# Optimization experiments

Measured on AMD Instinct MI355X. Metric: run time of the kernel, lower is better.

The kernel has to match this reference:

```python
import jax, jax.numpy as jnp
import numpy as np

E = 256
H = 8
DH = E // H
N = 200000
NEG = -1e9


def _normalize(x, eps=1e-12):
    # torch F.normalize: x / max(||x||_2, eps) along last dim
    n = jnp.linalg.norm(x, axis=-1, keepdims=True)
    return x / jnp.maximum(n, eps)


def setup_inputs() -> dict:
    key = jax.random.key(0)
    ks = jax.random.split(key, 16)
    s = 1.0 / np.sqrt(E)
    inp = {
        "context_vector": jax.random.normal(ks[0], (3 * E,), jnp.float32),
        "node_embeddings": jax.random.normal(ks[1], (N, E), jnp.float32),
        "invalid_action_mask": jax.random.randint(ks[2], (N,), 0, 2).astype(bool),
        # project_context: Linear(3E, E)
        "Wc": jax.random.normal(ks[3], (E, 3 * E), jnp.float32) * (1.0 / np.sqrt(3 * E)),
        "bc": jnp.zeros((E,), jnp.float32),
        # project_keys / project_values: Linear(E, E)
        "Wk": jax.random.normal(ks[4], (E, E), jnp.float32) * s,
        "bk": jnp.zeros((E,), jnp.float32),
        "Wv": jax.random.normal(ks[5], (E, E), jnp.float32) * s,
        "bv": jnp.zeros((E,), jnp.float32),
        # nn.MultiheadAttention packed in-projection and out-projection
        "in_proj_w": jax.random.normal(ks[6], (3 * E, E), jnp.float32) * s,
        "in_proj_b": jnp.zeros((3 * E,), jnp.float32),
        "out_proj_w": jax.random.normal(ks[7], (E, E), jnp.float32) * s,
        "out_proj_b": jnp.zeros((E,), jnp.float32),
        # project_attn_output: Linear(E, E)
        "Wo": jax.random.normal(ks[8], (E, E), jnp.float32) * s,
        "bo": jnp.zeros((E,), jnp.float32),
    }
    # guarantee at least one valid action
    inp["invalid_action_mask"] = inp["invalid_action_mask"].at[0].set(False)
    return inp


def reference(context_vector, node_embeddings, invalid_action_mask,
              Wc, bc, Wk, bk, Wv, bv,
              in_proj_w, in_proj_b, out_proj_w, out_proj_b, Wo, bo):
    valid = ~invalid_action_mask                        # [N]

    query = context_vector @ Wc.T + bc                  # [E]
    keys = _normalize(node_embeddings @ Wk.T + bk)      # [N, E]
    values = _normalize(node_embeddings @ Wv.T + bv)    # [N, E]

    # MultiheadAttention, single query, batch 1
    wq, wk2, wv2 = in_proj_w[:E], in_proj_w[E:2 * E], in_proj_w[2 * E:]
    bq, bk2, bv2 = in_proj_b[:E], in_proj_b[E:2 * E], in_proj_b[2 * E:]
    q = (query @ wq.T + bq).reshape(H, DH)              # [H, DH]
    k = (keys @ wk2.T + bk2).reshape(N, H, DH)          # [N, H, DH]
    v = (values @ wv2.T + bv2).reshape(N, H, DH)

    logits = jnp.einsum("hd,nhd->hn", q, k) / np.sqrt(DH)   # [H, N]
    logits = jnp.where(valid[None, :], logits, NEG)
    w = jax.nn.softmax(logits, axis=-1)                 # [H, N]
    attn = jnp.einsum("hn,nhd->hd", w, v).reshape(E)    # [E]
    attn = attn @ out_proj_w.T + out_proj_b             # [E]

    attn = _normalize(attn @ Wo.T + bo)                 # [E]

    # pointer scores over valid nodes (invalid -> prob 0)
    scores = jnp.where(valid, keys @ attn, NEG)         # [N]
    probs = jax.nn.softmax(scores)                      # [N]
    return probs
```

## Files before the change

### kernel.cpp

```cpp
#include <hip/hip_runtime.h>

#define NN 200000
#define NEGV -1000000000.0f

typedef __attribute__((ext_vector_type(8))) short bf16x8;
typedef __attribute__((ext_vector_type(4))) float f32x4;

__device__ __forceinline__ float bf2f(unsigned short u){
  unsigned int x = ((unsigned int)u) << 16;
  return __builtin_bit_cast(float, x);
}
__device__ __forceinline__ unsigned short f2bf(float f){
  unsigned int x = __builtin_bit_cast(unsigned int, f);
  x += 0x7fffu + ((x >> 16) & 1u);
  return (unsigned short)(x >> 16);
}
__device__ __forceinline__ void gload16(const void* g, void* l){
  __builtin_amdgcn_global_load_lds((const __attribute__((address_space(1))) unsigned int*)g,
                                   (__attribute__((address_space(3))) unsigned int*)l, 16, 0, 0);
}

static constexpr size_t OFF_RK     = 0;
static constexpr size_t OFF_RV     = 800256;
static constexpr size_t OFF_LOGITS = 1600512;
static constexpr size_t OFF_SCORES = 8000512;
static constexpr size_t OFF_QUERY  = 8800768;
static constexpr size_t OFF_Q2     = 8801792;
static constexpr size_t OFF_A2     = 8802816;
static constexpr size_t OFF_CONSTS = 8811008;
static constexpr size_t OFF_BIMG   = 8811264;
static constexpr size_t OFF_LSTAT  = 9081600;
static constexpr size_t OFF_MZ     = 9089792;
static constexpr size_t OFF_KATTN  = 9089856;
static constexpr size_t OFF_KB     = 9090880;
static constexpr size_t OFF_UPART  = 9090944;
static constexpr size_t OFF_TPART  = 13285248;
static constexpr size_t OFF_U      = 13301632;
static constexpr size_t OFF_T      = 13309824;
static constexpr size_t OFF_P3STAT = 13309888;
static constexpr size_t OFF_MZ3    = 13313984;
static constexpr size_t OFF_EMBBF  = 13314048;
static constexpr size_t WS_NEED_BF = OFF_EMBBF + (size_t)NN*512;

__global__ void k_query(const float* __restrict__ ctx, const float* __restrict__ Wc,
                        const float* __restrict__ bc, float* __restrict__ query){
  int e = blockIdx.x, t = threadIdx.x;
  float p = 0.f;
  #pragma unroll
  for (int r = 0; r < 3; r++){ int j = r*256 + t; p += ctx[j] * Wc[e*768 + j]; }
  #pragma unroll
  for (int m = 32; m; m >>= 1) p += __shfl_xor(p, m);
  __shared__ float red[4];
  if ((t & 63) == 0) red[t >> 6] = p;
  __syncthreads();
  if (t == 0) query[e] = red[0] + red[1] + red[2] + red[3] + bc[e];
}

__global__ void k_q2(const float* __restrict__ query, const float* __restrict__ ipw,
                     const float* __restrict__ ipb, float* __restrict__ q2){
  int d = blockIdx.x, t = threadIdx.x;
  float p = query[t] * ipw[d*256 + t];
  #pragma unroll
  for (int m = 32; m; m >>= 1) p += __shfl_xor(p, m);
  __shared__ float red[4];
  if ((t & 63) == 0) red[t >> 6] = p;
  __syncthreads();
  if (t == 0) q2[d] = red[0] + red[1] + red[2] + red[3] + ipb[d];
}

__global__ void k_AA(const float* __restrict__ q2, const float* __restrict__ ipw,
                     const float* __restrict__ ipb, const float* __restrict__ Wk,
                     const float* __restrict__ bk, float* __restrict__ A2,
                     float* __restrict__ consts){
  int h = blockIdx.x, t = threadIdx.x;
  __shared__ float qs[32];
  __shared__ float AHs[256];
  __shared__ float red[4];
  if (t < 32) qs[t] = q2[h*32 + t];
  __syncthreads();
  float a = 0.f;
  #pragma unroll
  for (int d = 0; d < 32; d++) a += qs[d] * ipw[(256 + h*32 + d)*256 + t];
  AHs[t] = a;
  if (t == 0){
    float ck = 0.f;
    for (int d = 0; d < 32; d++) ck += qs[d] * ipb[256 + h*32 + d];
    consts[8 + h] = ck;
  }
  __syncthreads();
  float a2 = 0.f;
  for (int e = 0; e < 256; e++) a2 += AHs[e] * Wk[e*256 + t];
  A2[h*256 + t] = a2;
  float cc = AHs[t] * bk[t];
  #pragma unroll
  for (int m = 32; m; m >>= 1) cc += __shfl_xor(cc, m);
  if ((t & 63) == 0) red[t >> 6] = cc;
  __syncthreads();
  if (t == 0) consts[h] = red[0] + red[1] + red[2] + red[3];
}

__global__ void k_bimg(const float* __restrict__ Wk, const float* __restrict__ Wv,
                       const float* __restrict__ A2, unsigned char* __restrict__ bimg){
  int g = blockIdx.x*256 + threadIdx.x;
  if (g >= 8*528*4) return;
  int s = g / (528*4);
  int rem = g % (528*4);
  int col = rem >> 2, kg = rem & 3;
  int j0 = s*32 + kg*8;
  const float* src = nullptr;
  if (col < 256) src = Wk + col*256 + j0;
  else if (col < 512) src = Wv + (col-256)*256 + j0;
  else if (col < 520) src = A2 + (col-512)*256 + j0;
  unsigned short u[8];
  #pragma unroll
  for (int i = 0; i < 8; i++) u[i] = src ? f2bf(src[i]) : (unsigned short)0;
  uint4 o;
  o.x = (unsigned int)u[0] | ((unsigned int)u[1] << 16);
  o.y = (unsigned int)u[2] | ((unsigned int)u[3] << 16);
  o.z = (unsigned int)u[4] | ((unsigned int)u[5] << 16);
  o.w = (unsigned int)u[6] | ((unsigned int)u[7] << 16);
  unsigned int addr = (unsigned int)((col*64 + kg*16) ^ ((col & 7) << 4));
  *(uint4*)(bimg + (size_t)s*33792 + addr) = o;
}

__launch_bounds__(256, 2)
__global__ void k_main(const float* __restrict__ emb, const unsigned char* __restrict__ bimg,
                       const int* __restrict__ mask, const float* __restrict__ consts,
                       float* __restrict__ rk_g, float* __restrict__ rv_g,
                       float* __restrict__ logits, unsigned char* __restrict__ ebf){
  __shared__ __align__(16) unsigned char smA[2][4096];
  __shared__ __align__(16) unsigned char smB[2][33792];
  __shared__ float sc_norm[4][64];
  __shared__ float rkbuf[64];
  const int tid = threadIdx.x;
  const int lane = tid & 63, wave = tid >> 6;
  const int c = lane & 15, kg = lane >> 4;
  const int nb0 = blockIdx.x * 64;

  auto stage = [&](int s, int buf){
    const unsigned char* bsrc = bimg + (size_t)s*33792;
    #pragma unroll
    for (int it = 0; it < 9; it++){
      int chunk = it*4 + wave;
      if (chunk < 33)
        gload16(bsrc + chunk*1024 + lane*16, &smB[buf][chunk*1024]);
    }
    int nl = tid >> 2, akg = tid & 3;
    const float* ap = emb + (size_t)(nb0 + nl)*256 + s*32 + akg*8;
    float4 f0 = *(const float4*)ap;
    float4 f1 = *(const float4*)(ap + 4);
    uint4 o;
    o.x = (unsigned int)f2bf(f0.x) | ((unsigned int)f2bf(f0.y) << 16);
    o.y = (unsigned int)f2bf(f0.z) | ((unsigned int)f2bf(f0.w) << 16);
    o.z = (unsigned int)f2bf(f1.x) | ((unsigned int)f2bf(f1.y) << 16);
    o.w = (unsigned int)f2bf(f1.z) | ((unsigned int)f2bf(f1.w) << 16);
    *(uint4*)&smA[buf][nl*64 + ((akg ^ ((nl >> 1) & 3)) << 4)] = o;
    if (ebf) *(uint4*)(ebf + (size_t)(nb0 + nl)*512 + s*64 + akg*16) = o;
  };

  f32x4 acc[4][9];
  #pragma unroll
  for (int st = 0; st < 4; st++)
    #pragma unroll
    for (int f = 0; f < 9; f++) acc[st][f] = (f32x4){0.f,0.f,0.f,0.f};

  stage(0, 0);
  for (int s = 0; s < 8; s++){
    int cur = s & 1;
    __syncthreads();
    if (s < 7) stage(s + 1, cur ^ 1);
    bf16x8 af[4];
    #pragma unroll
    for (int st = 0; st < 4; st++)
      af[st] = *(const bf16x8*)&smA[cur][st*1024 + c*64 + ((kg ^ ((c >> 1) & 3)) << 4)];
    #pragma unroll
    for (int f = 0; f < 9; f++){
      int cf = (f < 8) ? (wave*8 + f) : 32;
      bf16x8 bf = *(const bf16x8*)&smB[cur][(((cf*16 + c)*64 + kg*16)) ^ ((c & 7) << 4)];
      #pragma unroll
      for (int st = 0; st < 4; st++)
        acc[st][f] = __builtin_amdgcn_mfma_f32_16x16x32_bf16(af[st], bf, acc[st][f], 0, 0, 0);
    }
  }

  #pragma unroll
  for (int st = 0; st < 4; st++){
    #pragma unroll
    for (int i = 0; i < 4; i++){
      float p = 0.f;
      #pragma unroll
      for (int f = 0; f < 8; f++) p += acc[st][f][i]*acc[st][f][i];
      #pragma unroll
      for (int m = 1; m < 16; m <<= 1) p += __shfl_xor(p, m);
      if (c == 0) sc_norm[wave][st*16 + kg*4 + i] = p;
    }
  }
  __syncthreads();
  if (tid < 64){
    float pk = sc_norm[0][tid] + sc_norm[1][tid];
    float pv = sc_norm[2][tid] + sc_norm[3][tid];
    float rk = fmaxf(sqrtf(pk), 1e-12f);
    float rv = fmaxf(sqrtf(pv), 1e-12f);
    rk_g[nb0 + tid] = rk; rv_g[nb0 + tid] = rv;
    rkbuf[tid] = rk;
  }
  __syncthreads();
  if (wave == 3 && c < 8){
    const float rs32 = 0.17677669529663688f;
    float cb = consts[c], ck = consts[8 + c];
    #pragma unroll
    for (int st = 0; st < 4; st++){
      #pragma unroll
      for (int i = 0; i < 4; i++){
        int nl = st*16 + kg*4 + i;
        int n = nb0 + nl;
        float lg = (mask[n] == 0) ? ((acc[st][8][i] + cb)*rs32/rkbuf[nl] + ck*rs32) : NEGV;
        logits[(size_t)n*8 + c] = lg;
      }
    }
  }
}

__global__ void k_lstats(const float* __restrict__ logits, float* __restrict__ lstat){
  int tid = threadIdx.x;
  float m[8], z[8];
  #pragma unroll
  for (int h = 0; h < 8; h++){ m[h] = -3.0e38f; z[h] = 0.f; }
  for (int n = blockIdx.x*256 + tid; n < NN; n += 128*256){
    float4 a = *(const float4*)(logits + (size_t)n*8);
    float4 b = *(const float4*)(logits + (size_t)n*8 + 4);
    float l[8] = {a.x,a.y,a.z,a.w,b.x,b.y,b.z,b.w};
    #pragma unroll
    for (int h = 0; h < 8; h++){
      float M = fmaxf(m[h], l[h]);
      z[h] = z[h]*expf(m[h]-M) + expf(l[h]-M);
      m[h] = M;
    }
  }
  #pragma unroll
  for (int s = 1; s < 64; s <<= 1){
    #pragma unroll
    for (int h = 0; h < 8; h++){
      float m2 = __shfl_xor(m[h], s), z2 = __shfl_xor(z[h], s);
      float M = fmaxf(m[h], m2);
      z[h] = z[h]*expf(m[h]-M) + z2*expf(m2-M);
      m[h] = M;
    }
  }
  __shared__ float sm[4][8], sz[4][8];
  int wave = tid >> 6, lane = tid & 63;
  if (lane == 0){
    #pragma unroll
    for (int h = 0; h < 8; h++){ sm[wave][h] = m[h]; sz[wave][h] = z[h]; }
  }
  __syncthreads();
  if (tid < 8){
    float M = sm[0][tid], Z = sz[0][tid];
    #pragma unroll
    for (int w = 1; w < 4; w++){
      float M2 = fmaxf(M, sm[w][tid]);
      Z = Z*expf(M-M2) + sz[w][tid]*expf(sm[w][tid]-M2);
      M = M2;
    }
    lstat[(blockIdx.x*8 + tid)*2] = M;
    lstat[(blockIdx.x*8 + tid)*2 + 1] = Z;
  }
}

__global__ void k_mz(const float* __restrict__ lstat, float* __restrict__ MZ){
  int t = threadIdx.x;
  int h = t >> 3, seg = t & 7;
  float m = -3.0e38f, z = 0.f;
  for (int k = 0; k < 16; k++){
    int b = seg*16 + k;
    float m2 = lstat[(b*8 + h)*2], z2 = lstat[(b*8 + h)*2 + 1];
    float M = fmaxf(m, m2); z = z*expf(m-M) + z2*expf(m2-M); m = M;
  }
  #pragma unroll
  for (int s = 1; s < 8; s <<= 1){
    float m2 = __shfl_xor(m, s), z2 = __shfl_xor(z, s);
    float M = fmaxf(m, m2); z = z*expf(m-M) + z2*expf(m2-M); m = M;
  }
  if (seg == 0){ MZ[h] = m; MZ[8+h] = z; }
}

template<int BF>
__launch_bounds__(256)
__global__ void k_wsum(const void* __restrict__ embsrc, const float* __restrict__ logits,
                       const float* __restrict__ rv_g, const float* __restrict__ MZ,
                       float* __restrict__ upart, float* __restrict__ tpart){
  int tid = threadIdx.x, lane = tid & 63, wave = tid >> 6;
  int hl = lane & 31, h2 = lane >> 5;
  int gw = blockIdx.x*4 + wave;
  float Mh = MZ[hl & 7];
  float ua[8][8];
  #pragma unroll
  for (int h = 0; h < 8; h++)
    #pragma unroll
    for (int j = 0; j < 8; j++) ua[h][j] = 0.f;
  float tacc = 0.f;
  for (int p = gw; p < NN/2; p += 2048){
    int n = 2*p + h2;
    float e[8];
    if (BF){
      uint4 g = *(const uint4*)((const unsigned char*)embsrc + (size_t)n*512 + hl*16);
      e[0]=bf2f((unsigned short)(g.x&0xffff)); e[1]=bf2f((unsigned short)(g.x>>16));
      e[2]=bf2f((unsigned short)(g.y&0xffff)); e[3]=bf2f((unsigned short)(g.y>>16));
      e[4]=bf2f((unsigned short)(g.z&0xffff)); e[5]=bf2f((unsigned short)(g.z>>16));
      e[6]=bf2f((unsigned short)(g.w&0xffff)); e[7]=bf2f((unsigned short)(g.w>>16));
    } else {
      const float* ep = (const float*)embsrc + (size_t)n*256 + hl*8;
      float4 a = *(const float4*)ep, b = *(const float4*)(ep + 4);
      e[0]=a.x; e[1]=a.y; e[2]=a.z; e[3]=a.w; e[4]=b.x; e[5]=b.y; e[6]=b.z; e[7]=b.w;
    }
    float coef = 0.f;
    if (hl < 8) coef = expf(logits[(size_t)n*8 + hl] - Mh) / rv_g[n];
    tacc += coef;
    #pragma unroll
    for (int h = 0; h < 8; h++){
      float ch = __shfl(coef, h, 32);
      #pragma unroll
      for (int j = 0; j < 8; j++) ua[h][j] += ch * e[j];
    }
  }
  #pragma unroll
  for (int h = 0; h < 8; h++)
    #pragma unroll
    for (int j = 0; j < 8; j++) ua[h][j] += __shfl_xor(ua[h][j], 32);
  tacc += __shfl_xor(tacc, 32);
  __shared__ float ub[4][8][256];
  __shared__ float tb[4][8];
  if (h2 == 0){
    #pragma unroll
    for (int h = 0; h < 8; h++)
      #pragma unroll
      for (int j = 0; j < 8; j++) ub[wave][h][hl*8 + j] = ua[h][j];
    if (hl < 8) tb[wave][hl] = tacc;
  }
  __syncthreads();
  #pragma unroll
  for (int rep = 0; rep < 8; rep++){
    int idx = rep*256 + tid;
    int h = idx >> 8, j = idx & 255;
    upart[(size_t)blockIdx.x*2048 + h*256 + j] = ub[0][h][j]+ub[1][h][j]+ub[2][h][j]+ub[3][h][j];
  }
  if (tid < 8) tpart[blockIdx.x*8 + tid] = tb[0][tid]+tb[1][tid]+tb[2][tid]+tb[3][tid];
}

__global__ void k_ured(const float* __restrict__ upart, const float* __restrict__ tpart,
                       float* __restrict__ U, float* __restrict__ T){
  int h = blockIdx.x, j = threadIdx.x;
  float s = 0.f;
  for (int b = 0; b < 512; b++) s += upart[(size_t)b*2048 + h*256 + j];
  U[h*256 + j] = s;
  float tp = 0.f;
  if (j < 64){
    for (int i = 0; i < 8; i++) tp += tpart[(j*8 + i)*8 + h];
  }
  #pragma unroll
  for (int m = 1; m < 64; m <<= 1) tp += __shfl_xor(tp, m);
  if (j == 0) T[h] = tp;
}

__global__ void k_attn(const float* __restrict__ U, const float* __restrict__ T,
                       const float* __restrict__ MZ,
                       const float* __restrict__ Wv, const float* __restrict__ bv,
                       const float* __restrict__ ipw, const float* __restrict__ ipb,
                       const float* __restrict__ opw, const float* __restrict__ opb,
                       const float* __restrict__ Wo, const float* __restrict__ bo,
                       const float* __restrict__ Wk, const float* __restrict__ bk,
                       float* __restrict__ kattn, float* __restrict__ kbout){
  int t = threadIdx.x;
  __shared__ float u[8][256], sh[8][256];
  __shared__ float a1[256], o1[256], af[256];
  __shared__ float red[4];
  #pragma unroll
  for (int h = 0; h < 8; h++) u[h][t] = U[h*256 + t];
  __syncthreads();
  {
    float accs[8];
    #pragma unroll
    for (int h = 0; h < 8; h++) accs[h] = 0.f;
    for (int j = 0; j < 256; j++){
      float wv = Wv[t*256 + j];
      #pragma unroll
      for (int h = 0; h < 8; h++) accs[h] += wv * u[h][j];
    }
    #pragma unroll
    for (int h = 0; h < 8; h++) sh[h][t] = (accs[h] + bv[t]*T[h]) / MZ[8+h];
  }
  __syncthreads();
  {
    int h = t >> 5;
    float a = 0.f;
    for (int j = 0; j < 256; j++) a += ipw[(512 + t)*256 + j] * sh[h][j];
    a1[t] = a + ipb[512 + t];
  }
  __syncthreads();
  { float a = 0.f; for (int j = 0; j < 256; j++) a += opw[t*256 + j]*a1[j]; o1[t] = a + opb[t]; }
  __syncthreads();
  float o2v;
  { float a = 0.f; for (int j = 0; j < 256; j++) a += Wo[t*256 + j]*o1[j]; o2v = a + bo[t]; }
  {
    float sq = o2v*o2v;
    #pragma unroll
    for (int m = 1; m < 64; m <<= 1) sq += __shfl_xor(sq, m);
    if ((t & 63) == 0) red[t >> 6] = sq;
    __syncthreads();
    float nrm = fmaxf(sqrtf(red[0]+red[1]+red[2]+red[3]), 1e-12f);
    af[t] = o2v / nrm;
  }
  __syncthreads();
  { float a = 0.f; for (int e = 0; e < 256; e++) a += af[e]*Wk[e*256 + t]; kattn[t] = a; }
  {
    float cc = af[t]*bk[t];
    #pragma unroll
    for (int m = 1; m < 64; m <<= 1) cc += __shfl_xor(cc, m);
    __syncthreads();
    if ((t & 63) == 0) red[t >> 6] = cc;
    __syncthreads();
    if (t == 0) kbout[0] = red[0]+red[1]+red[2]+red[3];
  }
}

template<int BF>
__launch_bounds__(256)
__global__ void k_scores(const void* __restrict__ embsrc, const float* __restrict__ rk_g,
                         const int* __restrict__ mask, const float* __restrict__ kattn,
                         const float* __restrict__ kbp, float* __restrict__ scores,
                         float* __restrict__ p3stat){
  int tid = threadIdx.x, lane = tid & 63, wave = tid >> 6;
  int hl = lane & 31, h2 = lane >> 5;
  __shared__ float ka[256];
  ka[tid] = kattn[tid];
  __syncthreads();
  float kb = kbp[0];
  float kv[8];
  #pragma unroll
  for (int j = 0; j < 8; j++) kv[j] = ka[hl*8 + j];
  int gw = blockIdx.x*4 + wave;
  float m = -3.0e38f, z = 0.f;
  for (int p = gw; p < NN/2; p += 2048){
    int n = 2*p + h2;
    float d;
    if (BF){
      uint4 g = *(const uint4*)((const unsigned char*)embsrc + (size_t)n*512 + hl*16);
      d  = bf2f((unsigned short)(g.x&0xffff))*kv[0] + bf2f((unsigned short)(g.x>>16))*kv[1];
      d += bf2f((unsigned short)(g.y&0xffff))*kv[2] + bf2f((unsigned short)(g.y>>16))*kv[3];
      d += bf2f((unsigned short)(g.z&0xffff))*kv[4] + bf2f((unsigned short)(g.z>>16))*kv[5];
      d += bf2f((unsigned short)(g.w&0xffff))*kv[6] + bf2f((unsigned short)(g.w>>16))*kv[7];
    } else {
      const float* ep = (const float*)embsrc + (size_t)n*256 + hl*8;
      float4 a = *(const float4*)ep, b = *(const float4*)(ep + 4);
      d = a.x*kv[0]+a.y*kv[1]+a.z*kv[2]+a.w*kv[3]+b.x*kv[4]+b.y*kv[5]+b.z*kv[6]+b.w*kv[7];
    }
    #pragma unroll
    for (int s = 1; s < 32; s <<= 1) d += __shfl_xor(d, s);
    if (hl == 0){
      float sc = (mask[n] == 0) ? ((d + kb) / rk_g[n]) : NEGV;
      scores[n] = sc;
      float M = fmaxf(m, sc);
      z = z*expf(m - M) + expf(sc - M);
      m = M;
    }
  }
  float m2 = __shfl_xor(m, 32), z2 = __shfl_xor(z, 32);
  float M = fmaxf(m, m2); z = z*expf(m-M) + z2*expf(m2-M); m = M;
  __shared__ float rm[4], rz[4];
  if (lane == 0){ rm[wave] = m; rz[wave] = z; }
  __syncthreads();
  if (tid == 0){
    float Mx = rm[0], Z = rz[0];
    for (int w = 1; w < 4; w++){
      float M2 = fmaxf(Mx, rm[w]);
      Z = Z*expf(Mx - M2) + rz[w]*expf(rm[w] - M2);
      Mx = M2;
    }
    p3stat[blockIdx.x*2] = Mx; p3stat[blockIdx.x*2+1] = Z;
  }
}

__global__ void k_mz3(const float* __restrict__ p3stat, float* __restrict__ MZ3){
  int t = threadIdx.x;
  float m = p3stat[t*2], z = p3stat[t*2+1];
  {
    float m2 = p3stat[(t+256)*2], z2 = p3stat[(t+256)*2+1];
    float M = fmaxf(m, m2); z = z*expf(m-M) + z2*expf(m2-M); m = M;
  }
  #pragma unroll
  for (int mm = 1; mm < 64; mm <<= 1){
    float ms = __shfl_xor(m, mm), zs = __shfl_xor(z, mm);
    float Mx = fmaxf(m, ms); z = z*expf(m-Mx) + zs*expf(ms-Mx); m = Mx;
  }
  __shared__ float rm[4], rz[4];
  if ((t&63)==0){ rm[t>>6]=m; rz[t>>6]=z; }
  __syncthreads();
  if (t==0){
    float M=rm[0], Z=rz[0];
    for (int w=1; w<4; w++){ float Mx=fmaxf(M,rm[w]); Z=Z*expf(M-Mx)+rz[w]*expf(rm[w]-Mx); M=Mx; }
    MZ3[0]=M; MZ3[1]=Z;
  }
}

__global__ void k_probs(const float* __restrict__ scores, const float* __restrict__ MZ3,
                        float* __restrict__ out){
  float M = MZ3[0], iZ = 1.0f / MZ3[1];
  for (int n = blockIdx.x*256 + threadIdx.x; n < NN; n += 512*256)
    out[n] = expf(scores[n] - M) * iZ;
}

extern "C" void kernel_launch(void* const* d_in, const int* in_sizes, int n_in,
                              void* d_out, int out_size, void* d_ws, size_t ws_size,
                              hipStream_t stream){
  (void)in_sizes; (void)n_in; (void)out_size;
  const float* ctx = (const float*)d_in[0];
  const float* emb = (const float*)d_in[1];
  const int*   mask= (const int*)d_in[2];
  const float* Wc  = (const float*)d_in[3];
  const float* bc  = (const float*)d_in[4];
  const float* Wk  = (const float*)d_in[5];
  const float* bk  = (const float*)d_in[6];
  const float* Wv  = (const float*)d_in[7];
  const float* bv  = (const float*)d_in[8];
  const float* ipw = (const float*)d_in[9];
  const float* ipb = (const float*)d_in[10];
  const float* opw = (const float*)d_in[11];
  const float* opb = (const float*)d_in[12];
  const float* Wo  = (const float*)d_in[13];
  const float* bo  = (const float*)d_in[14];
  float* out = (float*)d_out;
  char* ws = (char*)d_ws;

  float* rk     = (float*)(ws + OFF_RK);
  float* rv     = (float*)(ws + OFF_RV);
  float* logits = (float*)(ws + OFF_LOGITS);
  float* scores = (float*)(ws + OFF_SCORES);
  float* query  = (float*)(ws + OFF_QUERY);
  float* q2     = (float*)(ws + OFF_Q2);
  float* A2     = (float*)(ws + OFF_A2);
  float* consts = (float*)(ws + OFF_CONSTS);
  unsigned char* bimg = (unsigned char*)(ws + OFF_BIMG);
  float* lstat  = (float*)(ws + OFF_LSTAT);
  float* MZ     = (float*)(ws + OFF_MZ);
  float* kattn  = (float*)(ws + OFF_KATTN);
  float* kb     = (float*)(ws + OFF_KB);
  float* upart  = (float*)(ws + OFF_UPART);
  float* tpart  = (float*)(ws + OFF_TPART);
  float* U      = (float*)(ws + OFF_U);
  float* T      = (float*)(ws + OFF_T);
  float* p3stat = (float*)(ws + OFF_P3STAT);
  float* MZ3    = (float*)(ws + OFF_MZ3);

  const bool bf = ws_size >= WS_NEED_BF;
  unsigned char* ebf = bf ? (unsigned char*)(ws + OFF_EMBBF) : nullptr;

  k_query <<<256, 256, 0, stream>>>(ctx, Wc, bc, query);
  k_q2    <<<256, 256, 0, stream>>>(query, ipw, ipb, q2);
  k_AA    <<<8,   256, 0, stream>>>(q2, ipw, ipb, Wk, bk, A2, consts);
  k_bimg  <<<66,  256, 0, stream>>>(Wk, Wv, A2, bimg);
  k_main  <<<3125,256, 0, stream>>>(emb, bimg, mask, consts, rk, rv, logits, ebf);
  k_lstats<<<128, 256, 0, stream>>>(logits, lstat);
  k_mz    <<<1,   64,  0, stream>>>(lstat, MZ);
  if (bf) k_wsum<1><<<512, 256, 0, stream>>>(ebf, logits, rv, MZ, upart, tpart);
  else    k_wsum<0><<<512, 256, 0, stream>>>(emb, logits, rv, MZ, upart, tpart);
  k_ured  <<<8,   256, 0, stream>>>(upart, tpart, U, T);
  k_attn  <<<1,   256, 0, stream>>>(U, T, MZ, Wv, bv, ipw, ipb, opw, opb, Wo, bo, Wk, bk, kattn, kb);
  if (bf) k_scores<1><<<512, 256, 0, stream>>>(ebf, rk, mask, kattn, kb, scores, p3stat);
  else    k_scores<0><<<512, 256, 0, stream>>>(emb, rk, mask, kattn, kb, scores, p3stat);
  k_mz3   <<<1,   256, 0, stream>>>(p3stat, MZ3);
  k_probs <<<512, 256, 0, stream>>>(scores, MZ3, out);
}
```

Before: 381.8 us.

## Fuse query prep kernels, warp-specialize main GEMM, parallelize reductions and attn matvecs

Merges the three tiny query/in-projection kernels into one single-block kernel to cut launch overhead. Rewrites the main MFMA kernel to use 512 threads, with four waves loading and converting embeddings (register-prefetched one stage ahead) and four waves staging the weight image, each wave now computing half the node tiles. Spreads the U reduction across 64 blocks instead of 8. Changes the single-block attention matvecs from per-thread row loops to coalesced wave-per-row dot products. The main kernel's higher thread count and new split may raise register or LDS pressure, and the prep kernel serializes work onto one block.

```diff
diff --git a/kernel.cpp b/kernel.cpp
--- a/kernel.cpp
+++ b/kernel.cpp
@@ -24,8 +24,6 @@
 static constexpr size_t OFF_RV     = 800256;
 static constexpr size_t OFF_LOGITS = 1600512;
 static constexpr size_t OFF_SCORES = 8000512;
-static constexpr size_t OFF_QUERY  = 8800768;
-static constexpr size_t OFF_Q2     = 8801792;
 static constexpr size_t OFF_A2     = 8802816;
 static constexpr size_t OFF_CONSTS = 8811008;
 static constexpr size_t OFF_BIMG   = 8811264;
@@ -42,61 +40,59 @@
 static constexpr size_t OFF_EMBBF  = 13314048;
 static constexpr size_t WS_NEED_BF = OFF_EMBBF + (size_t)NN*512;
 
-__global__ void k_query(const float* __restrict__ ctx, const float* __restrict__ Wc,
-                        const float* __restrict__ bc, float* __restrict__ query){
-  int e = blockIdx.x, t = threadIdx.x;
-  float p = 0.f;
-  #pragma unroll
-  for (int r = 0; r < 3; r++){ int j = r*256 + t; p += ctx[j] * Wc[e*768 + j]; }
-  #pragma unroll
-  for (int m = 32; m; m >>= 1) p += __shfl_xor(p, m);
-  __shared__ float red[4];
-  if ((t & 63) == 0) red[t >> 6] = p;
-  __syncthreads();
-  if (t == 0) query[e] = red[0] + red[1] + red[2] + red[3] + bc[e];
-}
-
-__global__ void k_q2(const float* __restrict__ query, const float* __restrict__ ipw,
-                     const float* __restrict__ ipb, float* __restrict__ q2){
-  int d = blockIdx.x, t = threadIdx.x;
-  float p = query[t] * ipw[d*256 + t];
-  #pragma unroll
-  for (int m = 32; m; m >>= 1) p += __shfl_xor(p, m);
-  __shared__ float red[4];
-  if ((t & 63) == 0) red[t >> 6] = p;
-  __syncthreads();
-  if (t == 0) q2[d] = red[0] + red[1] + red[2] + red[3] + ipb[d];
-}
-
-__global__ void k_AA(const float* __restrict__ q2, const float* __restrict__ ipw,
-                     const float* __restrict__ ipb, const float* __restrict__ Wk,
-                     const float* __restrict__ bk, float* __restrict__ A2,
-                     float* __restrict__ consts){
-  int h = blockIdx.x, t = threadIdx.x;
-  __shared__ float qs[32];
-  __shared__ float AHs[256];
-  __shared__ float red[4];
-  if (t < 32) qs[t] = q2[h*32 + t];
-  __syncthreads();
-  float a = 0.f;
-  #pragma unroll
-  for (int d = 0; d < 32; d++) a += qs[d] * ipw[(256 + h*32 + d)*256 + t];
-  AHs[t] = a;
-  if (t == 0){
-    float ck = 0.f;
-    for (int d = 0; d < 32; d++) ck += qs[d] * ipb[256 + h*32 + d];
-    consts[8 + h] = ck;
-  }
-  __syncthreads();
-  float a2 = 0.f;
-  for (int e = 0; e < 256; e++) a2 += AHs[e] * Wk[e*256 + t];
-  A2[h*256 + t] = a2;
-  float cc = AHs[t] * bk[t];
-  #pragma unroll
-  for (int m = 32; m; m >>= 1) cc += __shfl_xor(cc, m);
-  if ((t & 63) == 0) red[t >> 6] = cc;
-  __syncthreads();
-  if (t == 0) consts[h] = red[0] + red[1] + red[2] + red[3];
+__global__ void k_prep(const float* __restrict__ ctx, const float* __restrict__ Wc,
+                       const float* __restrict__ bc, const float* __restrict__ ipw,
+                       const float* __restrict__ ipb, const float* __restrict__ Wk,
+                       const float* __restrict__ bk, float* __restrict__ A2,
+                       float* __restrict__ consts){
+  int t = threadIdx.x, lane = t & 63, wave = t >> 6;
+  __shared__ float ctxs[768], querys[256], q2s[256], AHs[256];
+  __shared__ float red2[4], red3[4];
+  #pragma unroll
+  for (int r = 0; r < 3; r++) ctxs[r*256 + t] = ctx[r*256 + t];
+  __syncthreads();
+  for (int rr = 0; rr < 64; rr++){
+    int r = wave*64 + rr;
+    float d = 0.f;
+    #pragma unroll
+    for (int it = 0; it < 12; it++) d += ctxs[it*64 + lane] * Wc[r*768 + it*64 + lane];
+    #pragma unroll
+    for (int m = 1; m < 64; m <<= 1) d += __shfl_xor(d, m);
+    if (lane == 0) querys[r] = d + bc[r];
+  }
+  __syncthreads();
+  for (int rr = 0; rr < 64; rr++){
+    int r = wave*64 + rr;
+    float d = 0.f;
+    #pragma unroll
+    for (int it = 0; it < 4; it++) d += querys[it*64 + lane] * ipw[r*256 + it*64 + lane];
+    #pragma unroll
+    for (int m = 1; m < 64; m <<= 1) d += __shfl_xor(d, m);
+    if (lane == 0) q2s[r] = d + ipb[r];
+  }
+  __syncthreads();
+  for (int h = 0; h < 8; h++){
+    float a = 0.f;
+    #pragma unroll
+    for (int d = 0; d < 32; d++) a += q2s[h*32 + d] * ipw[(256 + h*32 + d)*256 + t];
+    __syncthreads();
+    AHs[t] = a;
+    float v = (t < 32) ? q2s[h*32 + t] * ipb[256 + h*32 + t] : 0.f;
+    #pragma unroll
+    for (int m = 1; m < 64; m <<= 1) v += __shfl_xor(v, m);
+    if (lane == 0) red2[wave] = v;
+    __syncthreads();
+    if (t == 0) consts[8 + h] = red2[0] + red2[1] + red2[2] + red2[3];
+    float a2 = 0.f;
+    for (int e = 0; e < 256; e++) a2 += AHs[e] * Wk[e*256 + t];
+    A2[h*256 + t] = a2;
+    float cc = AHs[t] * bk[t];
+    #pragma unroll
+    for (int m = 1; m < 64; m <<= 1) cc += __shfl_xor(cc, m);
+    if (lane == 0) red3[wave] = cc;
+    __syncthreads();
+    if (t == 0) consts[h] = red3[0] + red3[1] + red3[2] + red3[3];
+  }
 }
 
 __global__ void k_bimg(const float* __restrict__ Wk, const float* __restrict__ Wv,
@@ -123,96 +119,117 @@
   *(uint4*)(bimg + (size_t)s*33792 + addr) = o;
 }
 
-__launch_bounds__(256, 2)
+__launch_bounds__(512, 4)
 __global__ void k_main(const float* __restrict__ emb, const unsigned char* __restrict__ bimg,
                        const int* __restrict__ mask, const float* __restrict__ consts,
                        float* __restrict__ rk_g, float* __restrict__ rv_g,
                        float* __restrict__ logits, unsigned char* __restrict__ ebf){
   __shared__ __align__(16) unsigned char smA[2][4096];
   __shared__ __align__(16) unsigned char smB[2][33792];
-  __shared__ float sc_norm[4][64];
+  __shared__ float part[4][4][16];
   __shared__ float rkbuf[64];
   const int tid = threadIdx.x;
   const int lane = tid & 63, wave = tid >> 6;
+  const int sp = wave >> 2, ch = wave & 3;
   const int c = lane & 15, kg = lane >> 4;
   const int nb0 = blockIdx.x * 64;
-
-  auto stage = [&](int s, int buf){
-    const unsigned char* bsrc = bimg + (size_t)s*33792;
-    #pragma unroll
-    for (int it = 0; it < 9; it++){
-      int chunk = it*4 + wave;
-      if (chunk < 33)
-        gload16(bsrc + chunk*1024 + lane*16, &smB[buf][chunk*1024]);
-    }
-    int nl = tid >> 2, akg = tid & 3;
-    const float* ap = emb + (size_t)(nb0 + nl)*256 + s*32 + akg*8;
-    float4 f0 = *(const float4*)ap;
-    float4 f1 = *(const float4*)(ap + 4);
+  const bool isA = (wave < 4);
+  const int anode = tid >> 2, aq = tid & 3;
+  const int bw = wave - 4;
+
+  float4 qb0, qb1;
+
+  auto issueA = [&](int s){
+    const float* ap = emb + (size_t)(nb0 + anode)*256 + s*32 + aq*8;
+    qb0 = *(const float4*)ap;
+    qb1 = *(const float4*)(ap + 4);
+  };
+  auto writeFrom = [&](float4 f0, float4 f1, int s, int buf){
     uint4 o;
     o.x = (unsigned int)f2bf(f0.x) | ((unsigned int)f2bf(f0.y) << 16);
     o.y = (unsigned int)f2bf(f0.z) | ((unsigned int)f2bf(f0.w) << 16);
     o.z = (unsigned int)f2bf(f1.x) | ((unsigned int)f2bf(f1.y) << 16);
     o.w = (unsigned int)f2bf(f1.z) | ((unsigned int)f2bf(f1.w) << 16);
-    *(uint4*)&smA[buf][nl*64 + ((akg ^ ((nl >> 1) & 3)) << 4)] = o;
-    if (ebf) *(uint4*)(ebf + (size_t)(nb0 + nl)*512 + s*64 + akg*16) = o;
+    *(uint4*)&smA[buf][anode*64 + ((aq ^ ((anode >> 1) & 3)) << 4)] = o;
+    if (ebf) *(uint4*)(ebf + (size_t)(nb0 + anode)*512 + s*64 + aq*16) = o;
   };
-
-  f32x4 acc[4][9];
-  #pragma unroll
-  for (int st = 0; st < 4; st++)
+  auto stageB = [&](int s, int buf){
+    const unsigned char* bsrc = bimg + (size_t)s*33792;
+    #pragma unroll
+    for (int it = 0; it < 8; it++){
+      int chunk = bw*8 + it;
+      gload16(bsrc + chunk*1024 + lane*16, &smB[buf][chunk*1024]);
+    }
+    if (bw == 3) gload16(bsrc + 32*1024 + lane*16, &smB[buf][32768]);
+  };
+
+  f32x4 acc[2][9];
+  #pragma unroll
+  for (int st = 0; st < 2; st++)
     #pragma unroll
     for (int f = 0; f < 9; f++) acc[st][f] = (f32x4){0.f,0.f,0.f,0.f};
 
-  stage(0, 0);
+  if (isA){
+    const float* ap0 = emb + (size_t)(nb0 + anode)*256 + aq*8;
+    float4 qa0 = *(const float4*)ap0;
+    float4 qa1 = *(const float4*)(ap0 + 4);
+    issueA(1);
+    writeFrom(qa0, qa1, 0, 0);
+  } else {
+    stageB(0, 0);
+  }
+
   for (int s = 0; s < 8; s++){
     int cur = s & 1;
     __syncthreads();
-    if (s < 7) stage(s + 1, cur ^ 1);
-    bf16x8 af[4];
-    #pragma unroll
-    for (int st = 0; st < 4; st++)
-      af[st] = *(const bf16x8*)&smA[cur][st*1024 + c*64 + ((kg ^ ((c >> 1) & 3)) << 4)];
+    if (s < 7){
+      if (isA){
+        writeFrom(qb0, qb1, s + 1, cur ^ 1);
+        if (s + 2 <= 7) issueA(s + 2);
+      } else {
+        stageB(s + 1, cur ^ 1);
+      }
+    }
+    bf16x8 af0 = *(const bf16x8*)&smA[cur][(2*sp+0)*1024 + c*64 + ((kg ^ ((c >> 1) & 3)) << 4)];
+    bf16x8 af1 = *(const bf16x8*)&smA[cur][(2*sp+1)*1024 + c*64 + ((kg ^ ((c >> 1) & 3)) << 4)];
     #pragma unroll
     for (int f = 0; f < 9; f++){
-      int cf = (f < 8) ? (wave*8 + f) : 32;
-      bf16x8 bf = *(const bf16x8*)&smB[cur][(((cf*16 + c)*64 + kg*16)) ^ ((c & 7) << 4)];
-      #pragma unroll
-      for (int st = 0; st < 4; st++)
-        acc[st][f] = __builtin_amdgcn_mfma_f32_16x16x32_bf16(af[st], bf, acc[st][f], 0, 0, 0);
-    }
-  }
-
-  #pragma unroll
-  for (int st = 0; st < 4; st++){
+      int cf = (f < 8) ? (ch*8 + f) : 32;
+      bf16x8 bfv = *(const bf16x8*)&smB[cur][(((cf*16 + c)*64 + kg*16)) ^ ((c & 7) << 4)];
+      acc[0][f] = __builtin_amdgcn_mfma_f32_16x16x32_bf16(af0, bfv, acc[0][f], 0, 0, 0);
+      acc[1][f] = __builtin_amdgcn_mfma_f32_16x16x32_bf16(af1, bfv, acc[1][f], 0, 0, 0);
+    }
+  }
+
+  #pragma unroll
+  for (int st = 0; st < 2; st++){
     #pragma unroll
     for (int i = 0; i < 4; i++){
-      float p = 0.f;
-      #pragma unroll
-      for (int f = 0; f < 8; f++) p += acc[st][f][i]*acc[st][f][i];
-      #pragma unroll
-      for (int m = 1; m < 16; m <<= 1) p += __shfl_xor(p, m);
-      if (c == 0) sc_norm[wave][st*16 + kg*4 + i] = p;
+      float pp = 0.f;
+      #pragma unroll
+      for (int f = 0; f < 8; f++) pp += acc[st][f][i]*acc[st][f][i];
+      #pragma unroll
+      for (int m = 1; m < 16; m <<= 1) pp += __shfl_xor(pp, m);
+      if (c == 0) part[ch][2*sp + st][kg*4 + i] = pp;
     }
   }
   __syncthreads();
   if (tid < 64){
-    float pk = sc_norm[0][tid] + sc_norm[1][tid];
-    float pv = sc_norm[2][tid] + sc_norm[3][tid];
-    float rk = fmaxf(sqrtf(pk), 1e-12f);
-    float rv = fmaxf(sqrtf(pv), 1e-12f);
+    int gs = tid >> 4, r = tid & 15;
+    float rk = fmaxf(sqrtf(part[0][gs][r] + part[1][gs][r]), 1e-12f);
+    float rv = fmaxf(sqrtf(part[2][gs][r] + part[3][gs][r]), 1e-12f);
     rk_g[nb0 + tid] = rk; rv_g[nb0 + tid] = rv;
     rkbuf[tid] = rk;
   }
   __syncthreads();
-  if (wave == 3 && c < 8){
+  if (ch == 3 && c < 8){
     const float rs32 = 0.17677669529663688f;
     float cb = consts[c], ck = consts[8 + c];
     #pragma unroll
-    for (int st = 0; st < 4; st++){
+    for (int st = 0; st < 2; st++){
       #pragma unroll
       for (int i = 0; i < 4; i++){
-        int nl = st*16 + kg*4 + i;
+        int nl = (2*sp + st)*16 + kg*4 + i;
         int n = nb0 + nl;
         float lg = (mask[n] == 0) ? ((acc[st][8][i] + cb)*rs32/rkbuf[nl] + ck*rs32) : NEGV;
         logits[(size_t)n*8 + c] = lg;
@@ -349,17 +366,32 @@
 
 __global__ void k_ured(const float* __restrict__ upart, const float* __restrict__ tpart,
                        float* __restrict__ U, float* __restrict__ T){
-  int h = blockIdx.x, j = threadIdx.x;
+  int b = blockIdx.x; int h = b >> 3, js = b & 7;
+  int t = threadIdx.x; int j = js*32 + (t & 31); int br = t >> 5;
   float s = 0.f;
-  for (int b = 0; b < 512; b++) s += upart[(size_t)b*2048 + h*256 + j];
-  U[h*256 + j] = s;
-  float tp = 0.f;
-  if (j < 64){
-    for (int i = 0; i < 8; i++) tp += tpart[(j*8 + i)*8 + h];
-  }
-  #pragma unroll
-  for (int m = 1; m < 64; m <<= 1) tp += __shfl_xor(tp, m);
-  if (j == 0) T[h] = tp;
+  for (int k = 0; k < 64; k++){
+    int bb = k*8 + br;
+    s += upart[(size_t)bb*2048 + h*256 + j];
+  }
+  __shared__ float sb[8][32];
+  sb[br][t & 31] = s;
+  __syncthreads();
+  if (t < 32){
+    float tot = 0.f;
+    #pragma unroll
+    for (int r = 0; r < 8; r++) tot += sb[r][t];
+    U[h*256 + js*32 + t] = tot;
+  }
+  if (js == 0){
+    float tp = 0.f;
+    for (int i = t; i < 512; i += 256) tp += tpart[i*8 + h];
+    #pragma unroll
+    for (int m = 1; m < 64; m <<= 1) tp += __shfl_xor(tp, m);
+    __shared__ float rr[4];
+    if ((t & 63) == 0) rr[t >> 6] = tp;
+    __syncthreads();
+    if (t == 0) T[h] = rr[0]+rr[1]+rr[2]+rr[3];
+  }
 }
 
 __global__ void k_attn(const float* __restrict__ U, const float* __restrict__ T,
@@ -370,54 +402,88 @@
                        const float* __restrict__ Wo, const float* __restrict__ bo,
                        const float* __restrict__ Wk, const float* __restrict__ bk,
                        float* __restrict__ kattn, float* __restrict__ kbout){
-  int t = threadIdx.x;
-  __shared__ float u[8][256], sh[8][256];
-  __shared__ float a1[256], o1[256], af[256];
+  int t = threadIdx.x, lane = t & 63, wave = t >> 6;
+  __shared__ float u[8][256], sh2[8][256];
+  __shared__ float a1[256], o1[256], o2s[256], af[256];
   __shared__ float red[4];
   #pragma unroll
   for (int h = 0; h < 8; h++) u[h][t] = U[h*256 + t];
   __syncthreads();
+  for (int rr = 0; rr < 64; rr++){
+    int e = wave*64 + rr;
+    float acc8[8];
+    #pragma unroll
+    for (int h = 0; h < 8; h++) acc8[h] = 0.f;
+    #pragma unroll
+    for (int it = 0; it < 4; it++){
+      float wv = Wv[e*256 + it*64 + lane];
+      #pragma unroll
+      for (int h = 0; h < 8; h++) acc8[h] += wv * u[h][it*64 + lane];
+    }
+    #pragma unroll
+    for (int h = 0; h < 8; h++){
+      #pragma unroll
+      for (int m = 1; m < 64; m <<= 1) acc8[h] += __shfl_xor(acc8[h], m);
+    }
+    if (lane == 0){
+      float bve = bv[e];
+      #pragma unroll
+      for (int h = 0; h < 8; h++) sh2[h][e] = (acc8[h] + bve*T[h]) / MZ[8+h];
+    }
+  }
+  __syncthreads();
+  for (int rr = 0; rr < 64; rr++){
+    int e = wave*64 + rr;
+    int h = e >> 5;
+    float d = 0.f;
+    #pragma unroll
+    for (int it = 0; it < 4; it++) d += ipw[(512 + e)*256 + it*64 + lane] * sh2[h][it*64 + lane];
+    #pragma unroll
+    for (int m = 1; m < 64; m <<= 1) d += __shfl_xor(d, m);
+    if (lane == 0) a1[e] = d + ipb[512 + e];
+  }
+  __syncthreads();
+  for (int rr = 0; rr < 64; rr++){
+    int e = wave*64 + rr;
+    float d = 0.f;
+    #pragma unroll
+    for (int it = 0; it < 4; it++) d += opw[e*256 + it*64 + lane] * a1[it*64 + lane];
+    #pragma unroll
+    for (int m = 1; m < 64; m <<= 1) d += __shfl_xor(d, m);
+    if (lane == 0) o1[e] = d + opb[e];
+  }
+  __syncthreads();
+  for (int rr = 0; rr < 64; rr++){
+    int e = wave*64 + rr;
+    float d = 0.f;
+    #pragma unroll
+    for (int it = 0; it < 4; it++) d += Wo[e*256 + it*64 + lane] * o1[it*64 + lane];
+    #pragma unroll
+    for (int m = 1; m < 64; m <<= 1) d += __shfl_xor(d, m);
+    if (lane == 0) o2s[e] = d + bo[e];
+  }
+  __syncthreads();
   {
-    float accs[8];
-    #pragma unroll
-    for (int h = 0; h < 8; h++) accs[h] = 0.f;
-    for (int j = 0; j < 256; j++){
-      float wv = Wv[t*256 + j];
-      #pragma unroll
-      for (int h = 0; h < 8; h++) accs[h] += wv * u[h][j];
-    }
-    #pragma unroll
-    for (int h = 0; h < 8; h++) sh[h][t] = (accs[h] + bv[t]*T[h]) / MZ[8+h];
+    float sq = o2s[t]*o2s[t];
+    #pragma unroll
+    for (int m = 1; m < 64; m <<= 1) sq += __shfl_xor(sq, m);
+    if (lane == 0) red[wave] = sq;
+    __syncthreads();
+    float nrm = fmaxf(sqrtf(red[0]+red[1]+red[2]+red[3]), 1e-12f);
+    af[t] = o2s[t] / nrm;
   }
   __syncthreads();
   {
-    int h = t >> 5;
     float a = 0.f;
-    for (int j = 0; j < 256; j++) a += ipw[(512 + t)*256 + j] * sh[h][j];
-    a1[t] = a + ipb[512 + t];
-  }
-  __syncthreads();
-  { float a = 0.f; for (int j = 0; j < 256; j++) a += opw[t*256 + j]*a1[j]; o1[t] = a + opb[t]; }
-  __syncthreads();
-  float o2v;
-  { float a = 0.f; for (int j = 0; j < 256; j++) a += Wo[t*256 + j]*o1[j]; o2v = a + bo[t]; }
-  {
-    float sq = o2v*o2v;
-    #pragma unroll
-    for (int m = 1; m < 64; m <<= 1) sq += __shfl_xor(sq, m);
-    if ((t & 63) == 0) red[t >> 6] = sq;
-    __syncthreads();
-    float nrm = fmaxf(sqrtf(red[0]+red[1]+red[2]+red[3]), 1e-12f);
-    af[t] = o2v / nrm;
-  }
-  __syncthreads();
-  { float a = 0.f; for (int e = 0; e < 256; e++) a += af[e]*Wk[e*256 + t]; kattn[t] = a; }
+    for (int e = 0; e < 256; e++) a += af[e]*Wk[e*256 + t];
+    kattn[t] = a;
+  }
   {
     float cc = af[t]*bk[t];
     #pragma unroll
     for (int m = 1; m < 64; m <<= 1) cc += __shfl_xor(cc, m);
     __syncthreads();
-    if ((t & 63) == 0) red[t >> 6] = cc;
+    if (lane == 0) red[wave] = cc;
     __syncthreads();
     if (t == 0) kbout[0] = red[0]+red[1]+red[2]+red[3];
   }
@@ -535,8 +601,6 @@
   float* rv     = (float*)(ws + OFF_RV);
   float* logits = (float*)(ws + OFF_LOGITS);
   float* scores = (float*)(ws + OFF_SCORES);
-  float* query  = (float*)(ws + OFF_QUERY);
-  float* q2     = (float*)(ws + OFF_Q2);
   float* A2     = (float*)(ws + OFF_A2);
   float* consts = (float*)(ws + OFF_CONSTS);
   unsigned char* bimg = (unsigned char*)(ws + OFF_BIMG);
@@ -554,16 +618,14 @@
   const bool bf = ws_size >= WS_NEED_BF;
   unsigned char* ebf = bf ? (unsigned char*)(ws + OFF_EMBBF) : nullptr;
 
-  k_query <<<256, 256, 0, stream>>>(ctx, Wc, bc, query);
-  k_q2    <<<256, 256, 0, stream>>>(query, ipw, ipb, q2);
-  k_AA    <<<8,   256, 0, stream>>>(q2, ipw, ipb, Wk, bk, A2, consts);
+  k_prep  <<<1,   256, 0, stream>>>(ctx, Wc, bc, ipw, ipb, Wk, bk, A2, consts);
   k_bimg  <<<66,  256, 0, stream>>>(Wk, Wv, A2, bimg);
-  k_main  <<<3125,256, 0, stream>>>(emb, bimg, mask, consts, rk, rv, logits, ebf);
+  k_main  <<<3125,512, 0, stream>>>(emb, bimg, mask, consts, rk, rv, logits, ebf);
   k_lstats<<<128, 256, 0, stream>>>(logits, lstat);
   k_mz    <<<1,   64,  0, stream>>>(lstat, MZ);
   if (bf) k_wsum<1><<<512, 256, 0, stream>>>(ebf, logits, rv, MZ, upart, tpart);
   else    k_wsum<0><<<512, 256, 0, stream>>>(emb, logits, rv, MZ, upart, tpart);
-  k_ured  <<<8,   256, 0, stream>>>(upart, tpart, U, T);
+  k_ured  <<<64,  256, 0, stream>>>(upart, tpart, U, T);
   k_attn  <<<1,   256, 0, stream>>>(U, T, MZ, Wv, bv, ipw, ipb, opw, opb, Wo, bo, Wk, bk, kattn, kb);
   if (bf) k_scores<1><<<512, 256, 0, stream>>>(ebf, rk, mask, kattn, kb, scores, p3stat);
   else    k_scores<0><<<512, 256, 0, stream>>>(emb, rk, mask, kattn, kb, scores, p3stat);
```

New measurement: 835.5 us. +118.8%, slower.
